# Kernel tuning notes

Hardware: AMD Instinct MI355X
Metric: run time of the kernel (lower is better)

Reference implementation:

```python
import jax, jax.numpy as jnp
import numpy as np

# ---- module config (mirrors arch_args / init_kwargs) ----
W_BITS_PER_SLICE = 4      # slice_init=True -> weights quantized with STE to w_bits_per_slice
A_BITS = 8                # activation quantization bits
A_BITS_PER_STREAM = 8
VMAX = 1.0
GON_HW, GOFF_HW = 1.0, 1e-3   # weight_to_diff_conductance is called with Gon=1, Goff=1/1000 (hardcoded)
ADC_PREC = 8
ADC_STEP = 1e-3           # adc_static_step
NUM_SUBARRAYS = 9
SUB_SIZE = 256            # subarray_size; 256*3*3 / 256 = 9 even chunks
K, STRIDE, PAD = 3, 1, 1


def ste_quantize(x, bits):
    # Symmetric uniform quantizer with straight-through estimator (STE_Quantize).
    n = float(2 ** bits - 1)
    s = jnp.max(jnp.abs(x)) + 1e-12
    q = jnp.round(x / s * n) / n * s
    return x + jax.lax.stop_gradient(q - x)


def adc_quantize(I):
    # Nbit_ADC: static-step uniform ADC, signed (adc_pos_only=False), deterministic
    # rounding (adc_stoch_round=False), STE backward, no custom loss.
    half = 2 ** (ADC_PREC - 1)
    q = jnp.clip(jnp.round(I / ADC_STEP), -half, half - 1) * ADC_STEP
    return I + jax.lax.stop_gradient(q - I)


def setup_inputs():
    key = jax.random.key(0)
    k1, k2 = jax.random.split(key)
    x = jax.random.normal(k1, (32, 256, 32, 32), jnp.float32)
    fan_in = 256 * K * K
    w = jax.random.normal(k2, (256, 256, K, K), jnp.float32) * np.sqrt(2.0 / fan_in)  # kaiming_normal
    return {"inputs": x, "weight": w}


def reference(inputs, weight):
    B = inputs.shape[0]
    O = weight.shape[0]

    # forward(): quantize activations (a_bits) and weights (w_bits_per_slice, slice_init path)
    qa = ste_quantize(inputs, A_BITS)
    qw = ste_quantize(weight, W_BITS_PER_SLICE)

    # F.unfold -> [B, C*k*k, L], channel-major patch ordering (matches torch)
    patches = jax.lax.conv_general_dilated_patches(
        qa, (K, K), (STRIDE, STRIDE), ((PAD, PAD), (PAD, PAD)))
    Hp, Wp = patches.shape[2], patches.shape[3]
    L = Hp * Wp
    V = patches.reshape(B, NUM_SUBARRAYS, SUB_SIZE, L) * (VMAX / A_BITS_PER_STREAM)

    # Differential conductances: G_pos - G_neg. The dummy columns (both filled with
    # Goff) cancel exactly in I_pos - I_neg, so the net current per subarray is a
    # single contraction against qw * (Gon - Goff) / Nstates_slice.
    nstates = float(2 ** W_BITS_PER_SLICE - 1)
    Gd = qw.reshape(O, NUM_SUBARRAYS, SUB_SIZE) * ((GON_HW - GOFF_HW) / nstates)

    # per-subarray crossbar currents: [B, n_sub, O, L]
    I = jnp.einsum('bgfl,ogf->bgol', V, Gd)

    # shared ADC applied to each subarray output, then accumulate over subarrays
    accum = adc_quantize(I).sum(axis=1)  # [B, O, L]
    a_loss = jnp.float32(0.0)            # adc_custom_loss=False

    # F.fold with (1,1) kernel onto sqrt(L) x sqrt(L) grid == reshape
    result = accum.reshape(B, O, Hp, Wp)
    return (result, a_loss)
```

## Files before the change

### kernel.cpp

```cpp
#include <hip/hip_runtime.h>
#include <stdint.h>

typedef unsigned short u16;
typedef __attribute__((ext_vector_type(8))) short short8;
typedef __attribute__((ext_vector_type(4))) float floatx4;

#define NB 32
#define NC 256
#define NH 32
#define NW 32
#define NO 256
#define NPIX (NH*NW)
#define KPIX 9
#define NG 9
#define RUN 32
#define GK (NG*RUN)
#define KTOT (NG*GK)
#define PADH 34
#define PADSP (PADH*PADH)
#define QA_BSTRIDE (PADSP*NC)

#define AS1 __attribute__((address_space(1)))
#define AS3 __attribute__((address_space(3)))

__global__ void fused_pre(const float4* __restrict__ x4, int nx4,
                          const float4* __restrict__ w4, int nw4,
                          float* __restrict__ pmax, u16* __restrict__ qa) {
  int bid = blockIdx.x;
  if (bid >= 1088) {
    int zb = bid - 1088;
    int b = zb / 9;
    int rem = (zb % 9) * 256 + threadIdx.x;
    if (rem >= 2112) return;
    int pb = rem >> 4, c16 = rem & 15;
    int y, x;
    if (pb < 68) { y = (pb >= 34) ? 33 : 0; x = pb % 34; }
    else { int q = pb - 68; y = 1 + (q >> 1); x = (q & 1) ? 33 : 0; }
    uint4 z; z.x = z.y = z.z = z.w = 0u;
    *(uint4*)(qa + ((size_t)(b * PADH + y) * PADH + x) * NC + c16 * 16) = z;
    return;
  }
  const float4* p; int n4; int nb, b0;
  if (bid < 1024) { p = x4; n4 = nx4; nb = 1024; b0 = bid; }
  else            { p = w4; n4 = nw4; nb = 64;   b0 = bid - 1024; }
  float m = 0.f;
  for (int i = b0 * blockDim.x + threadIdx.x; i < n4; i += nb * blockDim.x) {
    float4 v = p[i];
    m = fmaxf(m, fmaxf(fmaxf(fabsf(v.x), fabsf(v.y)), fmaxf(fabsf(v.z), fabsf(v.w))));
  }
#pragma unroll
  for (int off = 32; off > 0; off >>= 1)
    m = fmaxf(m, __shfl_down(m, off, 64));
  __shared__ float sm[4];
  int lane = threadIdx.x & 63, wv = threadIdx.x >> 6;
  if (lane == 0) sm[wv] = m;
  __syncthreads();
  if (threadIdx.x == 0)
    pmax[bid] = fmaxf(fmaxf(sm[0], sm[1]), fmaxf(sm[2], sm[3]));
}

__device__ inline void reduce_pmax(const float* pmax, int tid, int nthreads,
                                   float* sred, float& mx_out, float& mw_out) {
  const float4* pf4 = (const float4*)pmax;
  float mx = 0.f, mw = 0.f;
  for (int t = tid; t < 256; t += nthreads) {
    float4 v = pf4[t];
    mx = fmaxf(mx, fmaxf(fmaxf(v.x, v.y), fmaxf(v.z, v.w)));
  }
  if (tid < 16) {
    float4 v = pf4[256 + tid];
    mw = fmaxf(fmaxf(v.x, v.y), fmaxf(v.z, v.w));
  }
#pragma unroll
  for (int off = 32; off > 0; off >>= 1) {
    mx = fmaxf(mx, __shfl_down(mx, off, 64));
    mw = fmaxf(mw, __shfl_down(mw, off, 64));
  }
  int lane = tid & 63, wv = tid >> 6, nw = nthreads >> 6;
  if (lane == 0) { sred[wv] = mx; sred[8 + wv] = mw; }
  __syncthreads();
  mx = sred[0]; mw = sred[8];
  for (int i = 1; i < nw; i++) { mx = fmaxf(mx, sred[i]); mw = fmaxf(mw, sred[8 + i]); }
  mx_out = mx; mw_out = mw;
}

__global__ void fused_quant(const float* __restrict__ x, const float* __restrict__ w,
                            const float* __restrict__ pmax,
                            u16* __restrict__ qa, u16* __restrict__ wq,
                            float* __restrict__ lossp) {
  __shared__ float sred[16];
  float mx, mw;
  reduce_pmax(pmax, threadIdx.x, 256, sred, mx, mw);
  int bid = blockIdx.x, tid = threadIdx.x;
  if (bid < 1024) {
    __shared__ u16 ts[32][264];
    double s = (double)mx + 1e-12;
    double inv = 255.0 / s;
    int b = bid >> 5, y = bid & 31;
    const float4* x4 = (const float4*)x;
    int xc = tid & 7, crow = tid >> 3;
#pragma unroll
    for (int it = 0; it < 8; it++) {
      int c = crow + 32 * it;
      float4 v = x4[((size_t)(b * NC + c) * NH + y) * 8 + xc];
      float q0 = (float)rint((double)v.x * inv);
      float q1 = (float)rint((double)v.y * inv);
      float q2 = (float)rint((double)v.z * inv);
      float q3 = (float)rint((double)v.w * inv);
      ts[xc * 4 + 0][c] = (u16)(__float_as_uint(q0) >> 16);
      ts[xc * 4 + 1][c] = (u16)(__float_as_uint(q1) >> 16);
      ts[xc * 4 + 2][c] = (u16)(__float_as_uint(q2) >> 16);
      ts[xc * 4 + 3][c] = (u16)(__float_as_uint(q3) >> 16);
    }
    __syncthreads();
    int xx = tid >> 3, qwl = tid & 7;
    u16* orow = qa + ((size_t)(b * PADH + y + 1) * PADH + (xx + 1)) * NC;
#pragma unroll
    for (int it = 0; it < 4; it++) {
      int qw = qwl + 8 * it;
      *(uint4*)(orow + qw * 8) = *(const uint4*)&ts[xx][qw * 8];
    }
    return;
  }
  double s = (double)mw + 1e-12;
  double inv = 15.0 / s;
  int idx = (bid - 1024) * 256 + tid;
  if (idx == 0) *lossp = 0.0f;
  int o = idx / KTOT, kk = idx % KTOT;
  int g = kk / GK, rem = kk % GK;
  int r = rem / RUN, j = rem % RUN;
  int clo = (256 * g - r + 8) / 9;
  int chi = (256 * (g + 1) - r + 8) / 9; if (chi > NC) chi = NC;
  int cst = ((256 * g) / 9) & ~3;
  int c = cst + j;
  float val = 0.f;
  if (c >= clo && c < chi) {
    float wv = w[((size_t)o * NC + c) * KPIX + r];
    val = (float)rint((double)wv * inv);
  }
  wq[idx] = (u16)(__float_as_uint(val) >> 16);
}

__global__ __launch_bounds__(512, 4) void gemm_adc(const u16* __restrict__ qa,
                                                   const u16* __restrict__ wq,
                                                   const float* __restrict__ pmax,
                                                   float* __restrict__ out) {
  __shared__ __align__(16) u16 lB[12288];
  __shared__ __align__(16) u16 sA[6528];
  __shared__ float sred[16];
  const int tid = threadIdx.x;
  float mx, mw;
  reduce_pmax(pmax, tid, 512, sred, mx, mw);

  const int mblk = blockIdx.x, nblk = blockIdx.y;
  const int b = mblk >> 3;
  const int p0 = (mblk & 7) * 128;
  const int y0 = (mblk & 7) * 4;
  const int n0 = nblk * 128;
  const int lane = tid & 63, wv = tid >> 6;
  const int wm = (wv & 1) * 64, wn = (wv >> 1) * 32;
  const int fm = lane & 15, fq = lane >> 4;
  const int swz = (fq + ((fm >> 1) & 3)) & 3;

  double sa = (double)mx + 1e-12;
  double sw = (double)mw + 1e-12;
  double Sstep = sa * sw * 0.999 / 459.0;

  const int OFS[9] = {0, 1, 2, 34, 35, 36, 68, 69, 70};
  int addrA[4][9];
#pragma unroll
  for (int mi = 0; mi < 4; mi++) {
    int pr = wm + mi * 16 + fm;
    int pixb = (pr >> 5) * 34 + (pr & 31);
#pragma unroll
    for (int t = 0; t < 9; t++) {
      int P = pixb + OFS[t];
      addrA[mi][t] = P * 32 + (((fq + ((P >> 1) & 3)) & 3) << 3);
    }
  }
  int bno[2];
#pragma unroll
  for (int ni = 0; ni < 2; ni++) bno[ni] = (wn + ni * 16 + fm) * RUN + swz * 8;

  const int jsrc = ((tid & 3) - ((tid >> 3) & 3)) & 3;
  const u16* Bb = wq + (size_t)(n0 + (tid >> 2)) * KTOT + jsrc * 8;

  const u16* Abase = qa + (size_t)b * QA_BSTRIDE + (size_t)y0 * PADH * NC;
  int soff[2], sdst[2];
#pragma unroll
  for (int i = 0; i < 2; i++) {
    int s = i * 512 + tid;
    soff[i] = (s >> 2) * NC + ((((s & 3) - ((s >> 3) & 3)) & 3) << 3);
    sdst[i] = s * 8;
  }

  floatx4 acc[4][2];
  float tot[4][2][4];
#pragma unroll
  for (int mi = 0; mi < 4; mi++)
#pragma unroll
    for (int ni = 0; ni < 2; ni++)
#pragma unroll
      for (int rr = 0; rr < 4; rr++) { acc[mi][ni][rr] = 0.f; tot[mi][ni][rr] = 0.f; }

  auto STAGE_SLAB = [&](int gp) {
    int cw = ((256 * gp) / 9) & ~3;
    const u16* srcg = Abase + cw;
    __builtin_amdgcn_global_load_lds((const AS1 void*)(srcg + soff[0]),
                                     (AS3 void*)&sA[sdst[0]], 16, 0, 0);
    if (tid < 304)
      __builtin_amdgcn_global_load_lds((const AS1 void*)(srcg + soff[1]),
                                       (AS3 void*)&sA[sdst[1]], 16, 0, 0);
  };
  auto STAGE_B = [&](int kb0) {
#pragma unroll
    for (int i = 0; i < 3; i++)
      __builtin_amdgcn_global_load_lds((const AS1 void*)(Bb + kb0 + i * RUN),
                                       (AS3 void*)&lB[(i * 512 + tid) * 8], 16, 0, 0);
  };
  auto FOLD = [&]() {
#pragma unroll
    for (int mi = 0; mi < 4; mi++)
#pragma unroll
      for (int ni = 0; ni < 2; ni++)
#pragma unroll
        for (int rr = 0; rr < 4; rr++) {
          double d = (double)acc[mi][ni][rr] * Sstep;
          float tf = (float)rint(d);
          tf = fminf(fmaxf(tf, -128.f), 127.f);
          tot[mi][ni][rr] += tf;
          acc[mi][ni][rr] = 0.f;
        }
  };

#pragma unroll 1
  for (int g = 0; g < NG; g++) {
    STAGE_SLAB(g);
    STAGE_B(g * GK);
    if (g > 0) FOLD();
#pragma unroll
    for (int rc = 0; rc < 3; rc++) {
      __syncthreads();
#pragma unroll
      for (int ri = 0; ri < 3; ri++) {
        short8 afr[4], bfr[2];
#pragma unroll
        for (int mi = 0; mi < 4; mi++)
          afr[mi] = *(const short8*)&sA[addrA[mi][rc * 3 + ri]];
#pragma unroll
        for (int ni = 0; ni < 2; ni++)
          bfr[ni] = *(const short8*)&lB[ri * 4096 + bno[ni]];
#pragma unroll
        for (int mi = 0; mi < 4; mi++)
#pragma unroll
          for (int ni = 0; ni < 2; ni++)
            acc[mi][ni] = __builtin_amdgcn_mfma_f32_16x16x32_bf16(afr[mi], bfr[ni], acc[mi][ni], 0, 0, 0);
      }
      __syncthreads();
      if (rc < 2) STAGE_B(g * GK + (rc + 1) * 96);
    }
  }
#pragma unroll
  for (int mi = 0; mi < 4; mi++)
#pragma unroll
    for (int ni = 0; ni < 2; ni++)
#pragma unroll
      for (int rr = 0; rr < 4; rr++) {
        double d = (double)acc[mi][ni][rr] * Sstep;
        float tf = (float)rint(d);
        tf = fminf(fmaxf(tf, -128.f), 127.f);
        tot[mi][ni][rr] += tf;
      }

#pragma unroll
  for (int mi = 0; mi < 4; mi++)
#pragma unroll
    for (int ni = 0; ni < 2; ni++) {
      int o = n0 + wn + ni * 16 + fm;
      int p = p0 + wm + mi * 16 + fq * 4;
      float4 o4;
      o4.x = tot[mi][ni][0] * 1e-3f;
      o4.y = tot[mi][ni][1] * 1e-3f;
      o4.z = tot[mi][ni][2] * 1e-3f;
      o4.w = tot[mi][ni][3] * 1e-3f;
      *(float4*)(out + ((size_t)(b * NO + o)) * NPIX + p) = o4;
    }
}

extern "C" void kernel_launch(void* const* d_in, const int* in_sizes, int n_in,
                              void* d_out, int out_size, void* d_ws, size_t ws_size,
                              hipStream_t stream) {
  const float* x = (const float*)d_in[0];
  const float* w = (const float*)d_in[1];
  float* out = (float*)d_out;

  float* pmax = (float*)d_ws;
  u16* qa = (u16*)((char*)d_ws + 8192);
  u16* wq = (u16*)((char*)d_ws + 8192 + 18939904 + 8192);

  fused_pre<<<1376, 256, 0, stream>>>((const float4*)x, (NB * NC * NH * NW) / 4,
                                      (const float4*)w, (NO * NC * KPIX) / 4,
                                      pmax, qa);
  fused_quant<<<1024 + 2592, 256, 0, stream>>>(x, w, pmax, qa, wq, out + (out_size - 1));
  gemm_adc<<<dim3(256, 2), 512, 0, stream>>>(qa, wq, pmax, out);
}
```

Measured before the change: 147.2 us.

## Load weight fragments directly from global and double-buffer activation slab

Drops the LDS staging of the weight tile. Each wave now reads its B fragments straight from global memory into registers. The activation slab is double-buffered in LDS, so the next subarray group is prefetched while the current one is computed. This removes most __syncthreads calls and the B-staging traffic, at the cost of exposed global-load latency on B inside the inner loop. Launch bounds drop to 2 blocks per CU, which changes occupancy and register allowance.

Result: slower. 196.7 us (+33.6%).

```diff
diff --git a/kernel.cpp b/kernel.cpp
--- a/kernel.cpp
+++ b/kernel.cpp
@@ -141,12 +141,11 @@
   wq[idx] = (u16)(__float_as_uint(val) >> 16);
 }
 
-__global__ __launch_bounds__(512, 4) void gemm_adc(const u16* __restrict__ qa,
+__global__ __launch_bounds__(512, 2) void gemm_adc(const u16* __restrict__ qa,
                                                    const u16* __restrict__ wq,
                                                    const float* __restrict__ pmax,
                                                    float* __restrict__ out) {
-  __shared__ __align__(16) u16 lB[12288];
-  __shared__ __align__(16) u16 sA[6528];
+  __shared__ __align__(16) u16 sA[13056];
   __shared__ float sred[16];
   const int tid = threadIdx.x;
   float mx, mw;
@@ -160,7 +159,6 @@
   const int lane = tid & 63, wv = tid >> 6;
   const int wm = (wv & 1) * 64, wn = (wv >> 1) * 32;
   const int fm = lane & 15, fq = lane >> 4;
-  const int swz = (fq + ((fm >> 1) & 3)) & 3;
 
   double sa = (double)mx + 1e-12;
   double sw = (double)mw + 1e-12;
@@ -178,12 +176,9 @@
       addrA[mi][t] = P * 32 + (((fq + ((P >> 1) & 3)) & 3) << 3);
     }
   }
-  int bno[2];
-#pragma unroll
-  for (int ni = 0; ni < 2; ni++) bno[ni] = (wn + ni * 16 + fm) * RUN + swz * 8;
-
-  const int jsrc = ((tid & 3) - ((tid >> 3) & 3)) & 3;
-  const u16* Bb = wq + (size_t)(n0 + (tid >> 2)) * KTOT + jsrc * 8;
+
+  const u16* bq0 = wq + (size_t)(n0 + wn + fm) * KTOT + fq * 8;
+  const u16* bq1 = bq0 + (size_t)16 * KTOT;
 
   const u16* Abase = qa + (size_t)b * QA_BSTRIDE + (size_t)y0 * PADH * NC;
   int soff[2], sdst[2];
@@ -205,18 +200,13 @@
 
   auto STAGE_SLAB = [&](int gp) {
     int cw = ((256 * gp) / 9) & ~3;
+    int ad = (gp & 1) * 6528;
     const u16* srcg = Abase + cw;
     __builtin_amdgcn_global_load_lds((const AS1 void*)(srcg + soff[0]),
-                                     (AS3 void*)&sA[sdst[0]], 16, 0, 0);
+                                     (AS3 void*)&sA[ad + sdst[0]], 16, 0, 0);
     if (tid < 304)
       __builtin_amdgcn_global_load_lds((const AS1 void*)(srcg + soff[1]),
-                                       (AS3 void*)&sA[sdst[1]], 16, 0, 0);
-  };
-  auto STAGE_B = [&](int kb0) {
-#pragma unroll
-    for (int i = 0; i < 3; i++)
-      __builtin_amdgcn_global_load_lds((const AS1 void*)(Bb + kb0 + i * RUN),
-                                       (AS3 void*)&lB[(i * 512 + tid) * 8], 16, 0, 0);
+                                       (AS3 void*)&sA[ad + sdst[1]], 16, 0, 0);
   };
   auto FOLD = [&]() {
 #pragma unroll
@@ -233,32 +223,30 @@
         }
   };
 
+  STAGE_SLAB(0);
+  __syncthreads();
+
 #pragma unroll 1
   for (int g = 0; g < NG; g++) {
-    STAGE_SLAB(g);
-    STAGE_B(g * GK);
+    const int ab = (g & 1) * 6528;
+    if (g < 8) STAGE_SLAB(g + 1);
     if (g > 0) FOLD();
 #pragma unroll
-    for (int rc = 0; rc < 3; rc++) {
-      __syncthreads();
-#pragma unroll
-      for (int ri = 0; ri < 3; ri++) {
-        short8 afr[4], bfr[2];
-#pragma unroll
-        for (int mi = 0; mi < 4; mi++)
-          afr[mi] = *(const short8*)&sA[addrA[mi][rc * 3 + ri]];
+    for (int r = 0; r < 9; r++) {
+      short8 afr[4], bfr[2];
+#pragma unroll
+      for (int mi = 0; mi < 4; mi++)
+        afr[mi] = *(const short8*)&sA[ab + addrA[mi][r]];
+      bfr[0] = *(const short8*)(bq0 + r * RUN);
+      bfr[1] = *(const short8*)(bq1 + r * RUN);
+#pragma unroll
+      for (int mi = 0; mi < 4; mi++)
 #pragma unroll
         for (int ni = 0; ni < 2; ni++)
-          bfr[ni] = *(const short8*)&lB[ri * 4096 + bno[ni]];
-#pragma unroll
-        for (int mi = 0; mi < 4; mi++)
-#pragma unroll
-          for (int ni = 0; ni < 2; ni++)
-            acc[mi][ni] = __builtin_amdgcn_mfma_f32_16x16x32_bf16(afr[mi], bfr[ni], acc[mi][ni], 0, 0, 0);
-      }
-      __syncthreads();
-      if (rc < 2) STAGE_B(g * GK + (rc + 1) * 96);
-    }
+          acc[mi][ni] = __builtin_amdgcn_mfma_f32_16x16x32_bf16(afr[mi], bfr[ni], acc[mi][ni], 0, 0, 0);
+    }
+    bq0 += GK; bq1 += GK;
+    __syncthreads();
   }
 #pragma unroll
   for (int mi = 0; mi < 4; mi++)
```
